# Optimization experiments

Hardware: AMD Instinct MI355X
Metric: run time of the kernel (lower is better)

## Reference

```python
import jax, jax.numpy as jnp
import numpy as np

DIM = 256
N_HEADS = 4
B, N = 2, 4096


def setup_inputs() -> dict:
    key = jax.random.key(0)
    ks = jax.random.split(key, 10)
    s = DIM ** -0.5
    return {
        "x": jax.random.normal(ks[0], (B, N, DIM), dtype=jnp.float32),
        "q_w": jax.random.normal(ks[1], (DIM, DIM), dtype=jnp.float32) * s,
        "q_b": jnp.zeros((DIM,), dtype=jnp.float32),
        "k_w": jax.random.normal(ks[2], (DIM, DIM), dtype=jnp.float32) * s,
        "k_b": jnp.zeros((DIM,), dtype=jnp.float32),
        "v_w": jax.random.normal(ks[3], (DIM, DIM), dtype=jnp.float32) * s,
        "v_b": jnp.zeros((DIM,), dtype=jnp.float32),
        "o_w": jax.random.normal(ks[4], (DIM, DIM), dtype=jnp.float32) * s,
        "o_b": jnp.zeros((DIM,), dtype=jnp.float32),
        "tau": jnp.ones((1,), dtype=jnp.float32),
    }


def reference(x, q_w, q_b, k_w, k_b, v_w, v_b, o_w, o_b, tau):
    Bsz, Nlen, C = x.shape
    H = N_HEADS
    Dh = C // H
    scale = C ** -0.5  # source uses full dim, not head_dim
    Q = (x @ q_w.T + q_b).reshape(Bsz, Nlen, H, Dh)
    K = (x @ k_w.T + k_b).reshape(Bsz, Nlen, H, Dh)
    V = (x @ v_w.T + v_b).reshape(Bsz, Nlen, H, Dh)
    attn = jnp.einsum('bnhd,bmhd->bhnm', Q, K) * scale
    # soft-threshold gate: keep only |attn| > tau, then relu
    attn = jax.nn.relu(jnp.where(jnp.abs(attn) > tau, attn, 0.0))
    attn = jax.nn.softmax(attn, axis=-1)
    out = jnp.einsum('bhnm,bmhd->bnhd', attn, V).reshape(Bsz, Nlen, C)
    return out @ o_w.T + o_b
```

## Files before the change

### kernel.cpp

```cpp
#include <hip/hip_runtime.h>

#define SEQ   4096
#define CDIM  256
#define NHEAD 4
#define DHEAD 64
#define PSTRIDE 72
#define NSPLIT 8

typedef float    f32x4 __attribute__((ext_vector_type(4)));
typedef _Float16 f16x8 __attribute__((ext_vector_type(8)));
typedef _Float16 f16x4 __attribute__((ext_vector_type(4)));

__device__ __forceinline__ f16x8 cvt_frag(const float* __restrict__ p) {
    float4 f0 = *(const float4*)p;
    float4 f1 = *(const float4*)(p + 4);
    f16x8 r;
    r[0]=(_Float16)f0.x; r[1]=(_Float16)f0.y; r[2]=(_Float16)f0.z; r[3]=(_Float16)f0.w;
    r[4]=(_Float16)f1.x; r[5]=(_Float16)f1.y; r[6]=(_Float16)f1.z; r[7]=(_Float16)f1.w;
    return r;
}

__global__ __launch_bounds__(256) void sta_prep(
    const float* __restrict__ qw, const float* __restrict__ kw,
    const float* __restrict__ vw, const float* __restrict__ ow,
    _Float16* __restrict__ w16)
{
    const int mat = blockIdx.y;
    const float* src = (mat == 0) ? qw : (mat == 1) ? kw : (mat == 2) ? vw : ow;
    const int i = (blockIdx.x * 256 + threadIdx.x) * 8;
    *(f16x8*)(w16 + mat * 65536 + i) = cvt_frag(src + i);
}

__global__ __launch_bounds__(256) void sta_qkv(
    const float* __restrict__ x, const _Float16* __restrict__ w16,
    const float* __restrict__ qb, const float* __restrict__ kb, const float* __restrict__ vb,
    _Float16* __restrict__ Qo, _Float16* __restrict__ Ko, _Float16* __restrict__ Vo)
{
    const int wave = threadIdx.x >> 6;
    const int lane = threadIdx.x & 63;
    const int l15  = lane & 15;
    const int quad = lane >> 4;
    const int mat  = blockIdx.y;
    const int half = blockIdx.z;
    const int row0 = blockIdx.x * 64 + wave * 16;

    const _Float16* w    = w16 + mat * 65536;
    const float*    bias = (mat == 0) ? qb : (mat == 1) ? kb : vb;

    f16x8 xf[8];
    const float* xrow = x + (row0 + l15) * CDIM + quad * 8;
    #pragma unroll
    for (int ks = 0; ks < 8; ks++) xf[ks] = cvt_frag(xrow + ks * 32);

    #pragma unroll 1
    for (int ct = 0; ct < 8; ct++) {
        const int ctg = half * 8 + ct;
        const _Float16* wr = w + (ctg * 16 + l15) * CDIM + quad * 8;
        f32x4 acc = {0.f, 0.f, 0.f, 0.f};
        if (mat < 2) {
            #pragma unroll
            for (int ks = 0; ks < 8; ks++)
                acc = __builtin_amdgcn_mfma_f32_16x16x32_f16(*(const f16x8*)(wr + ks * 32), xf[ks], acc, 0, 0, 0);
            const float4 bv = *(const float4*)(bias + ctg * 16 + quad * 4);
            const int c0 = ctg * 16 + quad * 4;
            const int h = c0 >> 6, d0 = c0 & 63;
            const int grow = row0 + l15, b = grow >> 12, n = grow & (SEQ - 1);
            const float sc = (mat == 0) ? 0.0625f : 1.0f;
            f16x4 o;
            o[0] = (_Float16)((acc[0] + bv.x) * sc);
            o[1] = (_Float16)((acc[1] + bv.y) * sc);
            o[2] = (_Float16)((acc[2] + bv.z) * sc);
            o[3] = (_Float16)((acc[3] + bv.w) * sc);
            _Float16* dst = ((mat == 0) ? Qo : Ko) + (((b * NHEAD + h) * SEQ + n) * DHEAD + d0);
            *(f16x4*)dst = o;
        } else {
            #pragma unroll
            for (int ks = 0; ks < 8; ks++)
                acc = __builtin_amdgcn_mfma_f32_16x16x32_f16(xf[ks], *(const f16x8*)(wr + ks * 32), acc, 0, 0, 0);
            const int c = ctg * 16 + l15;
            const int h = c >> 6, d = c & 63;
            const float bv = bias[c];
            const int grow0 = row0 + quad * 4, b = grow0 >> 12, n0 = grow0 & (SEQ - 1);
            f16x4 o;
            #pragma unroll
            for (int r = 0; r < 4; r++) o[r] = (_Float16)(acc[r] + bv);
            *(f16x4*)(Vo + (((b * NHEAD + h) * DHEAD + d) * SEQ + n0)) = o;
        }
    }
}

__global__ __launch_bounds__(64) void sta_attn(
    const _Float16* __restrict__ Q, const _Float16* __restrict__ K, const _Float16* __restrict__ Vt,
    const float* __restrict__ taup,
    _Float16* __restrict__ Opart, float* __restrict__ lfull)
{
    __shared__ __align__(16) _Float16 pbuf[64 * PSTRIDE];

    const int lane = threadIdx.x;
    const int l15  = lane & 15;
    const int quad = lane >> 4;
    const int qt = blockIdx.x;
    const int bh = blockIdx.y;
    const int sp = blockIdx.z;
    const float tau_eff = fmaxf(taup[0], 0.0f);

    const _Float16* Qb = Q  + bh * SEQ * DHEAD;
    const _Float16* Kb = K  + bh * SEQ * DHEAD;
    const _Float16* Vb = Vt + bh * DHEAD * SEQ;

    const int q0 = qt * 64;

    f16x8 qf[4][2];
    #pragma unroll
    for (int qb = 0; qb < 4; qb++)
        #pragma unroll
        for (int ks = 0; ks < 2; ks++)
            qf[qb][ks] = *(const f16x8*)(Qb + (q0 + qb * 16 + l15) * DHEAD + ks * 32 + quad * 8);

    f32x4 O[4][4];
    #pragma unroll
    for (int qb = 0; qb < 4; qb++)
        #pragma unroll
        for (int db = 0; db < 4; db++) O[qb][db] = (f32x4){0.f, 0.f, 0.f, 0.f};
    float rs[4] = {0.f, 0.f, 0.f, 0.f};

    #pragma unroll 1
    for (int kt = sp * 8; kt < sp * 8 + 8; kt++) {
        const int kv0 = kt * 64;

        #pragma unroll
        for (int kb = 0; kb < 4; kb++) {
            const _Float16* kp = Kb + (kv0 + kb * 16 + l15) * DHEAD + quad * 8;
            f16x8 k0 = *(const f16x8*)kp;
            f16x8 k1 = *(const f16x8*)(kp + 32);
            #pragma unroll
            for (int qb = 0; qb < 4; qb++) {
                f32x4 a = {0.f, 0.f, 0.f, 0.f};
                a = __builtin_amdgcn_mfma_f32_16x16x32_f16(k0, qf[qb][0], a, 0, 0, 0);
                a = __builtin_amdgcn_mfma_f32_16x16x32_f16(k1, qf[qb][1], a, 0, 0, 0);
                f16x4 pk;
                float acc = 0.f;
                #pragma unroll
                for (int r = 0; r < 4; r++) {
                    float e = __expf(a[r]);
                    float p = (a[r] > tau_eff) ? e : 1.0f;
                    acc += p;
                    pk[r] = (_Float16)p;
                }
                rs[qb] += acc;
                *(f16x4*)(pbuf + (qb * 16 + l15) * PSTRIDE + kb * 16 + quad * 4) = pk;
            }
        }

        #pragma unroll
        for (int ks = 0; ks < 2; ks++) {
            f16x8 pb[4];
            #pragma unroll
            for (int qb = 0; qb < 4; qb++)
                pb[qb] = *(const f16x8*)(pbuf + (qb * 16 + l15) * PSTRIDE + ks * 32 + quad * 8);
            #pragma unroll
            for (int db = 0; db < 4; db++) {
                f16x8 vf = *(const f16x8*)(Vb + (db * 16 + l15) * SEQ + kv0 + ks * 32 + quad * 8);
                #pragma unroll
                for (int qb = 0; qb < 4; qb++)
                    O[qb][db] = __builtin_amdgcn_mfma_f32_16x16x32_f16(vf, pb[qb], O[qb][db], 0, 0, 0);
            }
        }
    }

    #pragma unroll
    for (int qb = 0; qb < 4; qb++) {
        float v = rs[qb];
        v += __shfl_xor(v, 16);
        v += __shfl_xor(v, 32);
        rs[qb] = v;
    }
    _Float16* Ob = Opart + (size_t)((sp * 8 + bh) * SEQ + q0) * DHEAD;
    #pragma unroll
    for (int qb = 0; qb < 4; qb++) {
        #pragma unroll
        for (int db = 0; db < 4; db++) {
            f16x4 ov;
            #pragma unroll
            for (int r = 0; r < 4; r++) ov[r] = (_Float16)O[qb][db][r];
            *(f16x4*)(Ob + (qb * 16 + l15) * DHEAD + db * 16 + quad * 4) = ov;
        }
    }
    if (quad == 0) {
        #pragma unroll
        for (int qb = 0; qb < 4; qb++)
            atomicAdd(&lfull[bh * SEQ + q0 + qb * 16 + l15], rs[qb]);
    }
}

__global__ __launch_bounds__(128) void sta_oproj(
    const _Float16* __restrict__ Opart, const float* __restrict__ lfull,
    const _Float16* __restrict__ w16o, const float* __restrict__ ob,
    float* __restrict__ out)
{
    const int wave = threadIdx.x >> 6;
    const int lane = threadIdx.x & 63;
    const int l15  = lane & 15;
    const int quad = lane >> 4;
    const int row0 = blockIdx.x * 32 + wave * 16;
    const int quarter = blockIdx.y;

    const int grow = row0 + l15;
    const int b = grow >> 12, n = grow & (SEQ - 1);

    _Float16 inv[NHEAD];
    #pragma unroll
    for (int h = 0; h < NHEAD; h++)
        inv[h] = (_Float16)(1.0f / lfull[(b * NHEAD + h) * SEQ + n]);

    f16x8 af[8];
    #pragma unroll
    for (int ks = 0; ks < 8; ks++) {
        const int hq = ks * 4 + quad;
        const int h  = hq >> 3;
        const int d0 = (hq & 7) * 8;
        const _Float16* pp = Opart + (size_t)((b * NHEAD + h) * SEQ + n) * DHEAD + d0;
        f16x8 s = *(const f16x8*)pp;
        #pragma unroll
        for (int sp = 1; sp < NSPLIT; sp++)
            s = s + *(const f16x8*)(pp + (size_t)sp * 8 * SEQ * DHEAD);
        af[ks] = s * inv[h];
    }

    #pragma unroll 1
    for (int ct = 0; ct < 4; ct++) {
        const int ctg = quarter * 4 + ct;
        const _Float16* wr = w16o + (ctg * 16 + l15) * CDIM + quad * 8;
        f32x4 acc = {0.f, 0.f, 0.f, 0.f};
        #pragma unroll
        for (int ks = 0; ks < 8; ks++)
            acc = __builtin_amdgcn_mfma_f32_16x16x32_f16(*(const f16x8*)(wr + ks * 32), af[ks], acc, 0, 0, 0);
        const float4 bv = *(const float4*)(ob + ctg * 16 + quad * 4);
        const int c0 = ctg * 16 + quad * 4;
        float4 res;
        res.x = acc[0] + bv.x; res.y = acc[1] + bv.y;
        res.z = acc[2] + bv.z; res.w = acc[3] + bv.w;
        *(float4*)(out + (size_t)grow * CDIM + c0) = res;
    }
}

extern "C" void kernel_launch(void* const* d_in, const int* in_sizes, int n_in,
                              void* d_out, int out_size, void* d_ws, size_t ws_size,
                              hipStream_t stream) {
    const float* x   = (const float*)d_in[0];
    const float* qw  = (const float*)d_in[1];
    const float* qb  = (const float*)d_in[2];
    const float* kw  = (const float*)d_in[3];
    const float* kb  = (const float*)d_in[4];
    const float* vw  = (const float*)d_in[5];
    const float* vb  = (const float*)d_in[6];
    const float* ow  = (const float*)d_in[7];
    const float* ob  = (const float*)d_in[8];
    const float* tau = (const float*)d_in[9];

    _Float16* w16 = (_Float16*)d_ws;
    _Float16* Q   = w16 + 262144;
    _Float16* K   = Q + 2097152;
    _Float16* Vt  = K + 2097152;
    _Float16* Opart = Vt + 2097152;
    float* lfull  = (float*)(Opart + 16777216);

    sta_prep <<<dim3(32, 4),     256, 0, stream>>>(qw, kw, vw, ow, w16);
    sta_qkv  <<<dim3(128, 3, 2), 256, 0, stream>>>(x, w16, qb, kb, vb, Q, K, Vt);
    hipMemsetAsync(lfull, 0, NHEAD * 2 * SEQ * sizeof(float), stream);
    sta_attn <<<dim3(64, 8, 8),   64, 0, stream>>>(Q, K, Vt, tau, Opart, lfull);
    sta_oproj<<<dim3(256, 4),    128, 0, stream>>>(Opart, lfull, w16 + 3 * 65536, ob, (float*)d_out);
}
```

Measured before the change: 221.7 us.

## Drop weight prep kernel and memset, halve KV splits, use exp2 and fp32 partials

```diff
diff --git a/kernel.cpp b/kernel.cpp
--- a/kernel.cpp
+++ b/kernel.cpp
@@ -5,7 +5,8 @@
 #define NHEAD 4
 #define DHEAD 64
 #define PSTRIDE 72
-#define NSPLIT 8
+#define NSPLIT 4
+#define LOG2E 1.44269504f
 
 typedef float    f32x4 __attribute__((ext_vector_type(4)));
 typedef _Float16 f16x8 __attribute__((ext_vector_type(8)));
@@ -20,20 +21,11 @@
     return r;
 }
 
-__global__ __launch_bounds__(256) void sta_prep(
-    const float* __restrict__ qw, const float* __restrict__ kw,
-    const float* __restrict__ vw, const float* __restrict__ ow,
-    _Float16* __restrict__ w16)
-{
-    const int mat = blockIdx.y;
-    const float* src = (mat == 0) ? qw : (mat == 1) ? kw : (mat == 2) ? vw : ow;
-    const int i = (blockIdx.x * 256 + threadIdx.x) * 8;
-    *(f16x8*)(w16 + mat * 65536 + i) = cvt_frag(src + i);
-}
-
 __global__ __launch_bounds__(256) void sta_qkv(
-    const float* __restrict__ x, const _Float16* __restrict__ w16,
-    const float* __restrict__ qb, const float* __restrict__ kb, const float* __restrict__ vb,
+    const float* __restrict__ x,
+    const float* __restrict__ qw, const float* __restrict__ qb,
+    const float* __restrict__ kw, const float* __restrict__ kb,
+    const float* __restrict__ vw, const float* __restrict__ vb,
     _Float16* __restrict__ Qo, _Float16* __restrict__ Ko, _Float16* __restrict__ Vo)
 {
     const int wave = threadIdx.x >> 6;
@@ -44,8 +36,8 @@
     const int half = blockIdx.z;
     const int row0 = blockIdx.x * 64 + wave * 16;
 
-    const _Float16* w    = w16 + mat * 65536;
-    const float*    bias = (mat == 0) ? qb : (mat == 1) ? kb : vb;
+    const float* w    = (mat == 0) ? qw : (mat == 1) ? kw : vw;
+    const float* bias = (mat == 0) ? qb : (mat == 1) ? kb : vb;
 
     f16x8 xf[8];
     const float* xrow = x + (row0 + l15) * CDIM + quad * 8;
@@ -55,17 +47,20 @@
     #pragma unroll 1
     for (int ct = 0; ct < 8; ct++) {
         const int ctg = half * 8 + ct;
-        const _Float16* wr = w + (ctg * 16 + l15) * CDIM + quad * 8;
+        const float* wr = w + (ctg * 16 + l15) * CDIM + quad * 8;
+        f16x8 wf[8];
+        #pragma unroll
+        for (int ks = 0; ks < 8; ks++) wf[ks] = cvt_frag(wr + ks * 32);
         f32x4 acc = {0.f, 0.f, 0.f, 0.f};
         if (mat < 2) {
             #pragma unroll
             for (int ks = 0; ks < 8; ks++)
-                acc = __builtin_amdgcn_mfma_f32_16x16x32_f16(*(const f16x8*)(wr + ks * 32), xf[ks], acc, 0, 0, 0);
+                acc = __builtin_amdgcn_mfma_f32_16x16x32_f16(wf[ks], xf[ks], acc, 0, 0, 0);
             const float4 bv = *(const float4*)(bias + ctg * 16 + quad * 4);
             const int c0 = ctg * 16 + quad * 4;
             const int h = c0 >> 6, d0 = c0 & 63;
             const int grow = row0 + l15, b = grow >> 12, n = grow & (SEQ - 1);
-            const float sc = (mat == 0) ? 0.0625f : 1.0f;
+            const float sc = (mat == 0) ? (0.0625f * LOG2E) : 1.0f;
             f16x4 o;
             o[0] = (_Float16)((acc[0] + bv.x) * sc);
             o[1] = (_Float16)((acc[1] + bv.y) * sc);
@@ -76,7 +71,7 @@
         } else {
             #pragma unroll
             for (int ks = 0; ks < 8; ks++)
-                acc = __builtin_amdgcn_mfma_f32_16x16x32_f16(xf[ks], *(const f16x8*)(wr + ks * 32), acc, 0, 0, 0);
+                acc = __builtin_amdgcn_mfma_f32_16x16x32_f16(xf[ks], wf[ks], acc, 0, 0, 0);
             const int c = ctg * 16 + l15;
             const int h = c >> 6, d = c & 63;
             const float bv = bias[c];
@@ -92,17 +87,18 @@
 __global__ __launch_bounds__(64) void sta_attn(
     const _Float16* __restrict__ Q, const _Float16* __restrict__ K, const _Float16* __restrict__ Vt,
     const float* __restrict__ taup,
-    _Float16* __restrict__ Opart, float* __restrict__ lfull)
+    float* __restrict__ Opart, float* __restrict__ lpart)
 {
     __shared__ __align__(16) _Float16 pbuf[64 * PSTRIDE];
 
     const int lane = threadIdx.x;
     const int l15  = lane & 15;
     const int quad = lane >> 4;
-    const int qt = blockIdx.x;
-    const int bh = blockIdx.y;
-    const int sp = blockIdx.z;
-    const float tau_eff = fmaxf(taup[0], 0.0f);
+    const int bx = blockIdx.x;
+    const int qt = bx >> 5;
+    const int bh = (bx >> 2) & 7;
+    const int sp = bx & 3;
+    const float tau_eff = fmaxf(taup[0], 0.0f) * LOG2E;
 
     const _Float16* Qb = Q  + bh * SEQ * DHEAD;
     const _Float16* Kb = K  + bh * SEQ * DHEAD;
@@ -125,8 +121,15 @@
     float rs[4] = {0.f, 0.f, 0.f, 0.f};
 
     #pragma unroll 1
-    for (int kt = sp * 8; kt < sp * 8 + 8; kt++) {
+    for (int kt = sp * 16; kt < sp * 16 + 16; kt++) {
         const int kv0 = kt * 64;
+
+        f16x8 vf[2][4];
+        #pragma unroll
+        for (int ks = 0; ks < 2; ks++)
+            #pragma unroll
+            for (int db = 0; db < 4; db++)
+                vf[ks][db] = *(const f16x8*)(Vb + (db * 16 + l15) * SEQ + kv0 + ks * 32 + quad * 8);
 
         #pragma unroll
         for (int kb = 0; kb < 4; kb++) {
@@ -142,7 +145,7 @@
                 float acc = 0.f;
                 #pragma unroll
                 for (int r = 0; r < 4; r++) {
-                    float e = __expf(a[r]);
+                    float e = exp2f(a[r]);
                     float p = (a[r] > tau_eff) ? e : 1.0f;
                     acc += p;
                     pk[r] = (_Float16)p;
@@ -154,17 +157,15 @@
 
         #pragma unroll
         for (int ks = 0; ks < 2; ks++) {
-            f16x8 pb[4];
+            f16x8 pfr[4];
             #pragma unroll
             for (int qb = 0; qb < 4; qb++)
-                pb[qb] = *(const f16x8*)(pbuf + (qb * 16 + l15) * PSTRIDE + ks * 32 + quad * 8);
-            #pragma unroll
-            for (int db = 0; db < 4; db++) {
-                f16x8 vf = *(const f16x8*)(Vb + (db * 16 + l15) * SEQ + kv0 + ks * 32 + quad * 8);
+                pfr[qb] = *(const f16x8*)(pbuf + (qb * 16 + l15) * PSTRIDE + ks * 32 + quad * 8);
+            #pragma unroll
+            for (int db = 0; db < 4; db++)
                 #pragma unroll
                 for (int qb = 0; qb < 4; qb++)
-                    O[qb][db] = __builtin_amdgcn_mfma_f32_16x16x32_f16(vf, pb[qb], O[qb][db], 0, 0, 0);
-            }
+                    O[qb][db] = __builtin_amdgcn_mfma_f32_16x16x32_f16(vf[ks][db], pfr[qb], O[qb][db], 0, 0, 0);
         }
     }
 
@@ -175,27 +176,22 @@
         v += __shfl_xor(v, 32);
         rs[qb] = v;
     }
-    _Float16* Ob = Opart + (size_t)((sp * 8 + bh) * SEQ + q0) * DHEAD;
-    #pragma unroll
-    for (int qb = 0; qb < 4; qb++) {
-        #pragma unroll
-        for (int db = 0; db < 4; db++) {
-            f16x4 ov;
-            #pragma unroll
-            for (int r = 0; r < 4; r++) ov[r] = (_Float16)O[qb][db][r];
-            *(f16x4*)(Ob + (qb * 16 + l15) * DHEAD + db * 16 + quad * 4) = ov;
-        }
-    }
+    float* Ob = Opart + (size_t)((sp * 8 + bh) * SEQ + q0) * DHEAD;
+    #pragma unroll
+    for (int qb = 0; qb < 4; qb++)
+        #pragma unroll
+        for (int db = 0; db < 4; db++)
+            *(f32x4*)(Ob + (qb * 16 + l15) * DHEAD + db * 16 + quad * 4) = O[qb][db];
     if (quad == 0) {
         #pragma unroll
         for (int qb = 0; qb < 4; qb++)
-            atomicAdd(&lfull[bh * SEQ + q0 + qb * 16 + l15], rs[qb]);
+            lpart[(sp * 8 + bh) * SEQ + q0 + qb * 16 + l15] = rs[qb];
     }
 }
 
 __global__ __launch_bounds__(128) void sta_oproj(
-    const _Float16* __restrict__ Opart, const float* __restrict__ lfull,
-    const _Float16* __restrict__ w16o, const float* __restrict__ ob,
+    const float* __restrict__ Opart, const float* __restrict__ lpart,
+    const float* __restrict__ ow, const float* __restrict__ ob,
     float* __restrict__ out)
 {
     const int wave = threadIdx.x >> 6;
@@ -208,10 +204,15 @@
     const int grow = row0 + l15;
     const int b = grow >> 12, n = grow & (SEQ - 1);
 
-    _Float16 inv[NHEAD];
-    #pragma unroll
-    for (int h = 0; h < NHEAD; h++)
-        inv[h] = (_Float16)(1.0f / lfull[(b * NHEAD + h) * SEQ + n]);
+    float inv[NHEAD];
+    #pragma unroll
+    for (int h = 0; h < NHEAD; h++) {
+        float l = 0.f;
+        #pragma unroll
+        for (int sp = 0; sp < NSPLIT; sp++)
+            l += lpart[(sp * 8 + b * NHEAD + h) * SEQ + n];
+        inv[h] = 1.0f / l;
+    }
 
     f16x8 af[8];
     #pragma unroll
@@ -219,22 +220,34 @@
         const int hq = ks * 4 + quad;
         const int h  = hq >> 3;
         const int d0 = (hq & 7) * 8;
-        const _Float16* pp = Opart + (size_t)((b * NHEAD + h) * SEQ + n) * DHEAD + d0;
-        f16x8 s = *(const f16x8*)pp;
-        #pragma unroll
-        for (int sp = 1; sp < NSPLIT; sp++)
-            s = s + *(const f16x8*)(pp + (size_t)sp * 8 * SEQ * DHEAD);
-        af[ks] = s * inv[h];
+        const float* pp = Opart + (size_t)((b * NHEAD + h) * SEQ + n) * DHEAD + d0;
+        float4 s0 = {0.f,0.f,0.f,0.f}, s1 = {0.f,0.f,0.f,0.f};
+        #pragma unroll
+        for (int sp = 0; sp < NSPLIT; sp++) {
+            const float* q = pp + (size_t)sp * 8 * SEQ * DHEAD;
+            float4 a0 = *(const float4*)q;
+            float4 a1 = *(const float4*)(q + 4);
+            s0.x += a0.x; s0.y += a0.y; s0.z += a0.z; s0.w += a0.w;
+            s1.x += a1.x; s1.y += a1.y; s1.z += a1.z; s1.w += a1.w;
+        }
+        const float iv = inv[h];
+        f16x8 r;
+        r[0]=(_Float16)(s0.x*iv); r[1]=(_Float16)(s0.y*iv); r[2]=(_Float16)(s0.z*iv); r[3]=(_Float16)(s0.w*iv);
+        r[4]=(_Float16)(s1.x*iv); r[5]=(_Float16)(s1.y*iv); r[6]=(_Float16)(s1.z*iv); r[7]=(_Float16)(s1.w*iv);
+        af[ks] = r;
     }
 
     #pragma unroll 1
     for (int ct = 0; ct < 4; ct++) {
         const int ctg = quarter * 4 + ct;
-        const _Float16* wr = w16o + (ctg * 16 + l15) * CDIM + quad * 8;
+        const float* wr = ow + (ctg * 16 + l15) * CDIM + quad * 8;
+        f16x8 wf[8];
+        #pragma unroll
+        for (int ks = 0; ks < 8; ks++) wf[ks] = cvt_frag(wr + ks * 32);
         f32x4 acc = {0.f, 0.f, 0.f, 0.f};
         #pragma unroll
         for (int ks = 0; ks < 8; ks++)
-            acc = __builtin_amdgcn_mfma_f32_16x16x32_f16(*(const f16x8*)(wr + ks * 32), af[ks], acc, 0, 0, 0);
+            acc = __builtin_amdgcn_mfma_f32_16x16x32_f16(wf[ks], af[ks], acc, 0, 0, 0);
         const float4 bv = *(const float4*)(ob + ctg * 16 + quad * 4);
         const int c0 = ctg * 16 + quad * 4;
         float4 res;
@@ -258,16 +271,13 @@
     const float* ob  = (const float*)d_in[8];
     const float* tau = (const float*)d_in[9];
 
-    _Float16* w16 = (_Float16*)d_ws;
-    _Float16* Q   = w16 + 262144;
+    _Float16* Q   = (_Float16*)d_ws;
     _Float16* K   = Q + 2097152;
     _Float16* Vt  = K + 2097152;
-    _Float16* Opart = Vt + 2097152;
-    float* lfull  = (float*)(Opart + 16777216);
-
-    sta_prep <<<dim3(32, 4),     256, 0, stream>>>(qw, kw, vw, ow, w16);
-    sta_qkv  <<<dim3(128, 3, 2), 256, 0, stream>>>(x, w16, qb, kb, vb, Q, K, Vt);
-    hipMemsetAsync(lfull, 0, NHEAD * 2 * SEQ * sizeof(float), stream);
-    sta_attn <<<dim3(64, 8, 8),   64, 0, stream>>>(Q, K, Vt, tau, Opart, lfull);
-    sta_oproj<<<dim3(256, 4),    128, 0, stream>>>(Opart, lfull, w16 + 3 * 65536, ob, (float*)d_out);
-}
+    float* Opart  = (float*)(Vt + 2097152);
+    float* lpart  = Opart + 8388608;
+
+    sta_qkv  <<<dim3(128, 3, 2), 256, 0, stream>>>(x, qw, qb, kw, kb, vw, vb, Q, K, Vt);
+    sta_attn <<<2048, 64, 0, stream>>>(Q, K, Vt, tau, Opart, lpart);
+    sta_oproj<<<dim3(256, 4), 128, 0, stream>>>(Opart, lpart, ow, ob, (float*)d_out);
+}
```

Measured after the change: 279.7 us. 26.2% more time.
